# Kernel optimization log

Hardware: AMD Instinct MI355X
Metric: run time of the kernel (lower is better)

The kernel has to match this reference:

```python
import jax, jax.numpy as jnp
import numpy as np
from jax import lax

B, H, W, C, G, K = 2, 64, 64, 256, 8, 9
CQ = C // 4  # PConv partial channels
HC = C // G  # head channels
PTS = np.array([[-1, -1], [-1, 0], [-1, 1], [0, -1], [0, 0], [0, 1],
                [1, -1], [1, 0], [1, 1]], np.float32)  # (K,2) as (dx,dy)


def setup_inputs() -> dict:
    key = jax.random.key(0)
    ks = jax.random.split(key, 13)
    n = lambda i, shp, s: jax.random.normal(ks[i], shp, jnp.float32) * s
    return {
        'x': jax.random.normal(ks[0], (B, H, W, C), jnp.float32),
        'qkv_w': n(1, (C, 3 * C), C ** -0.5),
        'qkv_b': n(2, (3 * C,), 0.02),
        'dw_w': n(3, (3, 3, 1, 3 * C), 1.0 / 3.0),
        'dw_b': n(4, (3 * C,), 0.02),
        'off_pconv_w': n(5, (G, CQ, CQ, 3, 3), (CQ * 9) ** -0.5),
        'off_w': n(6, (G, 2 * K, C), 0.1 * C ** -0.5),
        'off_b': n(7, (G, 2 * K), 0.1),
        'mask_pconv_w': n(8, (CQ, CQ, 3, 3), (CQ * 9) ** -0.5),
        'mask_w': n(9, (K, C), C ** -0.5),
        'mask_b': n(10, (K,), 0.02),
        'proj_w': n(11, (C, C), C ** -0.5),
        'proj_b': n(12, (C,), 0.02),
    }


def _dwconv_nhwc(x, w, b):
    # depthwise 3x3, pad 1, stride 1; x (B,H,W,ch), w (3,3,1,ch)
    ch = x.shape[-1]
    y = lax.conv_general_dilated(x, w, (1, 1), 'SAME',
                                 dimension_numbers=('NHWC', 'HWIO', 'NHWC'),
                                 feature_group_count=ch)
    return y + b


def _pconv_nchw(x, w):
    # partial conv: 3x3 (no bias) on first CQ channels, rest untouched
    dc = w.shape[0]
    x1 = lax.conv_general_dilated(x[:, :dc], w, (1, 1), 'SAME',
                                  dimension_numbers=('NCHW', 'OIHW', 'NCHW'))
    return jnp.concatenate([x1, x[:, dc:]], axis=1)


def _flow_warp(x, flow):
    # x (N,Cc,Hh,Ww), flow (N,2K,Hh,Ww) -> (N,Cc,K,Hh,Ww)
    # bilinear grid_sample, border padding, align_corners=True == sampling at
    # absolute pixel coords with coordinate clamping.
    N, Cc, Hh, Ww = x.shape
    Kk = flow.shape[1] // 2
    fl = flow.reshape(N, Kk, 2, Hh, Ww).transpose(0, 3, 4, 1, 2)  # (N,H,W,K,2)
    gy, gx = jnp.meshgrid(jnp.arange(Hh, dtype=x.dtype),
                          jnp.arange(Ww, dtype=x.dtype), indexing='ij')
    base = jnp.stack([gx, gy], axis=-1)  # (H,W,2) in (x,y) order
    coords = base[None, :, :, None, :] + fl  # (N,H,W,K,2)
    cx = jnp.clip(coords[..., 0], 0.0, Ww - 1)
    cy = jnp.clip(coords[..., 1], 0.0, Hh - 1)
    x0 = jnp.floor(cx)
    y0 = jnp.floor(cy)
    wx = (cx - x0).reshape(N, 1, -1)
    wy = (cy - y0).reshape(N, 1, -1)
    x0i = x0.astype(jnp.int32)
    y0i = y0.astype(jnp.int32)
    x1i = jnp.minimum(x0i + 1, Ww - 1)
    y1i = jnp.minimum(y0i + 1, Hh - 1)
    xf = x.reshape(N, Cc, Hh * Ww)

    def gather(yi, xi):
        idx = (yi * Ww + xi).reshape(N, -1)  # (N, H*W*K)
        return jax.vmap(lambda im, ix: im[:, ix])(xf, idx)  # (N,Cc,H*W*K)

    v00 = gather(y0i, x0i)
    v01 = gather(y0i, x1i)
    v10 = gather(y1i, x0i)
    v11 = gather(y1i, x1i)
    out = (v00 * (1 - wx) * (1 - wy) + v01 * wx * (1 - wy)
           + v10 * (1 - wx) * wy + v11 * wx * wy)
    return out.reshape(N, Cc, Hh, Ww, Kk).transpose(0, 1, 4, 2, 3)


def reference(x, qkv_w, qkv_b, dw_w, dw_b, off_pconv_w, off_w, off_b,
              mask_pconv_w, mask_w, mask_b, proj_w, proj_b):
    Bb, Hh, Ww, Cc = x.shape
    P = Hh * Ww
    scale = HC ** -0.5
    # qkv projection + depthwise conv (NHWC)
    qkv = x @ qkv_w + qkv_b                       # (B,H,W,3C)
    qkv = _dwconv_nhwc(qkv, dw_w, dw_b)
    q = qkv[..., :Cc]                             # (B,H,W,C)
    k_map = jnp.transpose(qkv[..., Cc:2 * Cc], (0, 3, 1, 2))   # (B,C,H,W)
    v_map = jnp.transpose(qkv[..., 2 * Cc:], (0, 3, 1, 2))     # (B,C,H,W)
    q_nchw = jnp.transpose(q, (0, 3, 1, 2))

    # shared mask conv: PConv + 1x1 -> (B,K,H,W)
    xm = _pconv_nchw(q_nchw, mask_pconv_w)
    mask = jnp.einsum('bchw,oc->bohw', xm, mask_w) + mask_b[None, :, None, None]

    # base offsets per group: points_pool * (2g+1), flattened (dx,dy) pairs
    base = jnp.asarray(np.stack([(PTS * (2 * g + 1)).reshape(-1)
                                 for g in range(G)], axis=0))  # (G,2K)

    k_list, v_list = [], []
    for g in range(G):
        xo = _pconv_nchw(q_nchw, off_pconv_w[g])
        off = (jnp.einsum('bchw,oc->bohw', xo, off_w[g])
               + off_b[g][None, :, None, None]
               + base[g][None, :, None, None])  # (B,2K,H,W)
        sl = slice(g * HC, (g + 1) * HC)
        k_list.append(_flow_warp(k_map[:, sl], off) * mask[:, None])
        v_list.append(_flow_warp(v_map[:, sl], off) * mask[:, None])

    # stack (G,B,hc,K,H,W) -> (B,G,P,K,hc)
    def arrange(lst):
        t = jnp.stack(lst, axis=0).transpose(1, 0, 4, 5, 3, 2)
        return t.reshape(Bb, G, P, K, HC)

    k = arrange(k_list)
    v = arrange(v_list)
    qh = (q.reshape(Bb, Hh, Ww, G, HC).transpose(0, 3, 1, 2, 4)
          .reshape(Bb, G, P, HC)) * scale

    attn = jnp.einsum('bgpc,bgpkc->bgpk', qh, k)
    attn = jax.nn.softmax(attn, axis=-1)
    out = jnp.einsum('bgpk,bgpkc->bgpc', attn, v)       # (B,G,P,hc)
    out = out.transpose(0, 2, 1, 3).reshape(Bb, Hh, Ww, Cc)
    return out @ proj_w + proj_b
```

## Files before the change

kernel.cpp:

```cpp
#include <hip/hip_runtime.h>

typedef unsigned short u16;
typedef unsigned int u32;
typedef short bf16x8 __attribute__((ext_vector_type(8)));
typedef float f32x4 __attribute__((ext_vector_type(4)));

#define PP 4096
#define KPT 9

__device__ __forceinline__ u16 f2b(float f) {
    union { float f; unsigned int u; } v; v.f = f;
    unsigned int u = v.u;
    unsigned int r = u + 0x7FFFu + ((u >> 16) & 1u);
    return (u16)(r >> 16);
}
__device__ __forceinline__ float b2f(u16 b) {
    union { unsigned int u; float f; } v; v.u = ((unsigned int)b) << 16;
    return v.f;
}

__global__ __launch_bounds__(256) void convert_inputs(
        const float* __restrict__ x, const float* __restrict__ qkv_w,
        const float* __restrict__ proj_w,
        u16* __restrict__ x_b, u16* __restrict__ qkv_wT_b, u16* __restrict__ proj_wT_b) {
    int idx = blockIdx.x * 256 + threadIdx.x;
    if (idx < 2097152) { x_b[idx] = f2b(x[idx]); return; }
    int i2 = idx - 2097152;
    if (i2 < 196608) {
        int r = i2 / 768, c = i2 % 768;
        qkv_wT_b[c * 256 + r] = f2b(qkv_w[i2]);
        return;
    }
    int i3 = i2 - 196608;
    int r = i3 >> 8, c = i3 & 255;
    proj_wT_b[c * 256 + r] = f2b(proj_w[i3]);
}

template<bool OUT_BF16>
__global__ __launch_bounds__(256) void mfma_gemm(
        const u16* __restrict__ A, const u16* __restrict__ BT,
        const float* __restrict__ bias, void* __restrict__ out,
        int M, int N, int K) {
    __shared__ u16 As[128][40];
    __shared__ u16 Bs[64][40];
    int tid = threadIdx.x;
    int row0 = blockIdx.x * 128, col0 = blockIdx.y * 64;
    int wid = tid >> 6, lane = tid & 63;
    int wr = wid >> 1, wc = wid & 1;
    int l15 = lane & 15, lhi = lane >> 4;
    f32x4 acc[4][2] = {};
    for (int k0 = 0; k0 < K; k0 += 32) {
        #pragma unroll
        for (int q = 0; q < 2; q++) {
            int idx = tid + q * 256;
            int r = idx >> 2, kc = (idx & 3) * 8;
            *(bf16x8*)&As[r][kc] = *(const bf16x8*)&A[(size_t)(row0 + r) * K + k0 + kc];
        }
        {
            int r = tid >> 2, kc = (tid & 3) * 8;
            *(bf16x8*)&Bs[r][kc] = *(const bf16x8*)&BT[(size_t)(col0 + r) * K + k0 + kc];
        }
        __syncthreads();
        bf16x8 bfr[2];
        #pragma unroll
        for (int j = 0; j < 2; j++)
            bfr[j] = *(const bf16x8*)&Bs[wc * 32 + j * 16 + l15][lhi * 8];
        #pragma unroll
        for (int i = 0; i < 4; i++) {
            bf16x8 afr = *(const bf16x8*)&As[wr * 64 + i * 16 + l15][lhi * 8];
            #pragma unroll
            for (int j = 0; j < 2; j++)
                acc[i][j] = __builtin_amdgcn_mfma_f32_16x16x32_bf16(afr, bfr[j], acc[i][j], 0, 0, 0);
        }
        __syncthreads();
    }
    #pragma unroll
    for (int i = 0; i < 4; i++) {
        int row = row0 + wr * 64 + i * 16 + lhi * 4;
        #pragma unroll
        for (int j = 0; j < 2; j++) {
            int col = col0 + wc * 32 + j * 16 + l15;
            float bv = bias[col];
            #pragma unroll
            for (int r = 0; r < 4; r++) {
                float v = acc[i][j][r] + bv;
                if (OUT_BF16) ((u16*)out)[(size_t)(row + r) * N + col] = f2b(v);
                else          ((float*)out)[(size_t)(row + r) * N + col] = v;
            }
        }
    }
}

__global__ __launch_bounds__(256) void dwconv_b(const u16* __restrict__ qkv_b,
        const float* __restrict__ dww, const float* __restrict__ dwb,
        u16* __restrict__ out) {
    int idx = blockIdx.x * 256 + threadIdx.x;
    int c8 = (idx % 96) * 8;
    int pix = idx / 96;
    int w = pix & 63, h = (pix >> 6) & 63, b = pix >> 12;
    float acc[8];
    #pragma unroll
    for (int j = 0; j < 8; j++) acc[j] = dwb[c8 + j];
    #pragma unroll
    for (int ky = 0; ky < 3; ky++) {
        int hh = h + ky - 1;
        if (hh < 0 || hh >= 64) continue;
        #pragma unroll
        for (int kx = 0; kx < 3; kx++) {
            int ww = w + kx - 1;
            if (ww < 0 || ww >= 64) continue;
            bf16x8 v = *(const bf16x8*)&qkv_b[((size_t)((b * 64 + hh) * 64 + ww)) * 768 + c8];
            #pragma unroll
            for (int j = 0; j < 8; j++)
                acc[j] += b2f((u16)v[j]) * dww[(ky * 3 + kx) * 768 + c8 + j];
        }
    }
    bf16x8 o;
    #pragma unroll
    for (int j = 0; j < 8; j++) o[j] = (short)f2b(acc[j]);
    *(bf16x8*)&out[(size_t)idx * 8] = o;
}

__global__ void make_cw(const float* __restrict__ off_pconv_w,
        const float* __restrict__ off_w, const float* __restrict__ off_b,
        const float* __restrict__ mask_pconv_w, const float* __restrict__ mask_w,
        const float* __restrict__ mask_b, u16* __restrict__ cwT_b,
        float* __restrict__ cb) {
    int k = blockIdx.x;
    int o = threadIdx.x;
    float val = 0.f;
    if (o < 153) {
        if (k < 576) {
            int patch = k >> 6, i = k & 63;
            if (o < 144) {
                int g = o / 18, oo = o % 18;
                for (int c = 0; c < 64; c++)
                    val += off_w[(g * 18 + oo) * 256 + c] *
                           off_pconv_w[((g * 64 + c) * 64 + i) * 9 + patch];
            } else {
                int oo = o - 144;
                for (int c = 0; c < 64; c++)
                    val += mask_w[oo * 256 + c] * mask_pconv_w[(c * 64 + i) * 9 + patch];
            }
        } else {
            int j = k - 576;
            if (o < 144) {
                int g = o / 18, oo = o % 18;
                val = off_w[(g * 18 + oo) * 256 + 64 + j];
            } else {
                val = mask_w[(o - 144) * 256 + 64 + j];
            }
        }
    }
    cwT_b[o * 768 + k] = f2b(val);
    if (k == 0) {
        float bv = 0.f;
        if (o < 144) {
            int g = o / 18, oo = o % 18;
            const float PTSf[18] = {-1,-1,-1,0,-1,1,0,-1,0,0,0,1,1,-1,1,0,1,1};
            bv = off_b[g * 18 + oo] + PTSf[oo] * (float)(2 * g + 1);
        } else if (o < 153) {
            bv = mask_b[o - 144];
        }
        cb[o] = bv;
    }
}

__global__ __launch_bounds__(256) void offmask_mfma(const u16* __restrict__ qdw_b,
        const u16* __restrict__ cwT_b, const float* __restrict__ cb,
        float* __restrict__ offmask) {
    __shared__ u16 As[32][40];
    __shared__ u16 Bs[160][40];
    int tid = threadIdx.x;
    int p0 = blockIdx.x * 32;
    int wid = tid >> 6, lane = tid & 63;
    int wr = wid >> 1, wc = wid & 1;
    int l15 = lane & 15, lhi = lane >> 4;
    f32x4 acc[5] = {};
    for (int k0 = 0; k0 < 768; k0 += 32) {
        if (tid < 128) {
            int r = tid >> 2, kc = (tid & 3) * 8;
            int pixel = p0 + r;
            int w = pixel & 63, h = (pixel >> 6) & 63, b = pixel >> 12;
            bf16x8 v = {};
            if (k0 < 576) {
                int patch = k0 >> 6;
                int dy = patch / 3 - 1, dx = patch % 3 - 1;
                int hh = h + dy, ww = w + dx;
                if (hh >= 0 && hh < 64 && ww >= 0 && ww < 64)
                    v = *(const bf16x8*)&qdw_b[((size_t)((b * 64 + hh) * 64 + ww)) * 768 + (k0 & 63) + kc];
            } else {
                v = *(const bf16x8*)&qdw_b[((size_t)((b * 64 + h) * 64 + w)) * 768 + 64 + (k0 - 576) + kc];
            }
            *(bf16x8*)&As[r][kc] = v;
        }
        for (int idx = tid; idx < 640; idx += 256) {
            int r = idx >> 2, kc = (idx & 3) * 8;
            *(bf16x8*)&Bs[r][kc] = *(const bf16x8*)&cwT_b[r * 768 + k0 + kc];
        }
        __syncthreads();
        bf16x8 afr = *(const bf16x8*)&As[wr * 16 + l15][lhi * 8];
        #pragma unroll
        for (int j = 0; j < 5; j++) {
            bf16x8 bfr = *(const bf16x8*)&Bs[wc * 80 + j * 16 + l15][lhi * 8];
            acc[j] = __builtin_amdgcn_mfma_f32_16x16x32_bf16(afr, bfr, acc[j], 0, 0, 0);
        }
        __syncthreads();
    }
    int row = p0 + wr * 16 + lhi * 4;
    #pragma unroll
    for (int j = 0; j < 5; j++) {
        int col = wc * 80 + j * 16 + l15;
        float bv = cb[col];
        #pragma unroll
        for (int r = 0; r < 4; r++)
            offmask[(size_t)(row + r) * 160 + col] = acc[j][r] + bv;
    }
}

__global__ __launch_bounds__(256) void precompute_pts(const float* __restrict__ offmask,
        float4* __restrict__ pre) {
    int idx = blockIdx.x * 256 + threadIdx.x;
    if (idx >= 2 * PP * 72) return;
    int item = idx % 72;
    int pix = idx / 72;
    int g = item / 9, k = item % 9;
    int w = pix & 63, h = (pix >> 6) & 63;
    const float* om = offmask + (size_t)pix * 160;
    float dx = om[g * 18 + 2 * k];
    float dy = om[g * 18 + 2 * k + 1];
    float m  = om[144 + k];
    float cx = fminf(fmaxf((float)w + dx, 0.f), 63.f);
    float cy = fminf(fmaxf((float)h + dy, 0.f), 63.f);
    float x0f = floorf(cx), y0f = floorf(cy);
    int x0 = (int)x0f, y0 = (int)y0f;
    u32 idx00 = (u32)((pix & ~4095) | (y0 << 6) | x0);
    u32 pk = idx00 | ((x0 < 63) ? 0x10000u : 0u) | ((y0 < 63) ? 0x20000u : 0u);
    float4 o;
    o.x = __uint_as_float(pk);
    o.y = cx - x0f;
    o.z = cy - y0f;
    o.w = m;
    pre[idx] = o;
}

__global__ __launch_bounds__(256) void deform_attn(const u16* __restrict__ qdw_b,
        const float4* __restrict__ pre, u16* __restrict__ attn_b) {
    int tid = threadIdx.x;
    int unit = blockIdx.x * 16 + (tid >> 4);
    int cl = tid & 15;
    int b = unit >> 15;
    int g = (unit >> 12) & 7;
    int p = unit & 4095;
    int pix = (b << 12) | p;
    const float scale = 0.17677669529663687f;
    u32 qu = *(const u32*)&qdw_b[(size_t)pix * 768 + g * 32 + 2 * cl];
    float qlo = __uint_as_float(qu << 16) * scale;
    float qhi = __uint_as_float(qu & 0xFFFF0000u) * scale;
    const float4* pp = pre + (size_t)pix * 72 + g * 9;
    const char* base = (const char*)qdw_b;
    u32 ckb = (u32)(512 + (g * 32 + 2 * cl) * 2);
    float logit[KPT], vlo[KPT], vhi[KPT];
    #pragma unroll
    for (int k_ = 0; k_ < KPT; k_++) {
        float4 q4 = pp[k_];
        u32 pk = __float_as_uint(q4.x);
        float wx = q4.y, wy = q4.z, m = q4.w;
        u32 o00 = (pk & 0xFFFFu) * 1536u + ckb;
        u32 dX = (pk & 0x10000u) ? 1536u : 0u;
        u32 dY = (pk & 0x20000u) ? 98304u : 0u;
        u32 o01 = o00 + dX, o10 = o00 + dY, o11 = o00 + dY + dX;
        u32 k00 = *(const u32*)(base + o00);
        u32 v00 = *(const u32*)(base + o00 + 512);
        u32 k01 = *(const u32*)(base + o01);
        u32 v01 = *(const u32*)(base + o01 + 512);
        u32 k10 = *(const u32*)(base + o10);
        u32 v10 = *(const u32*)(base + o10 + 512);
        u32 k11 = *(const u32*)(base + o11);
        u32 v11 = *(const u32*)(base + o11 + 512);
        float w00 = (1.f - wx) * (1.f - wy), w01 = wx * (1.f - wy);
        float w10 = (1.f - wx) * wy,         w11 = wx * wy;
        float klo = __uint_as_float(k00 << 16) * w00 + __uint_as_float(k01 << 16) * w01
                  + __uint_as_float(k10 << 16) * w10 + __uint_as_float(k11 << 16) * w11;
        float khi = __uint_as_float(k00 & 0xFFFF0000u) * w00 + __uint_as_float(k01 & 0xFFFF0000u) * w01
                  + __uint_as_float(k10 & 0xFFFF0000u) * w10 + __uint_as_float(k11 & 0xFFFF0000u) * w11;
        float Vlo = __uint_as_float(v00 << 16) * w00 + __uint_as_float(v01 << 16) * w01
                  + __uint_as_float(v10 << 16) * w10 + __uint_as_float(v11 << 16) * w11;
        float Vhi = __uint_as_float(v00 & 0xFFFF0000u) * w00 + __uint_as_float(v01 & 0xFFFF0000u) * w01
                  + __uint_as_float(v10 & 0xFFFF0000u) * w10 + __uint_as_float(v11 & 0xFFFF0000u) * w11;
        float part = qlo * klo + qhi * khi;
        part += __shfl_xor(part, 8);
        part += __shfl_xor(part, 4);
        part += __shfl_xor(part, 2);
        part += __shfl_xor(part, 1);
        logit[k_] = part * m;
        vlo[k_] = Vlo * m;
        vhi[k_] = Vhi * m;
    }
    float mx = logit[0];
    #pragma unroll
    for (int k_ = 1; k_ < KPT; k_++) mx = fmaxf(mx, logit[k_]);
    float s = 0.f;
    #pragma unroll
    for (int k_ = 0; k_ < KPT; k_++) { logit[k_] = expf(logit[k_] - mx); s += logit[k_]; }
    float inv = 1.f / s;
    float olo = 0.f, ohi = 0.f;
    #pragma unroll
    for (int k_ = 0; k_ < KPT; k_++) { olo += logit[k_] * vlo[k_]; ohi += logit[k_] * vhi[k_]; }
    olo *= inv; ohi *= inv;
    u32 outw = (u32)f2b(olo) | ((u32)f2b(ohi) << 16);
    *(u32*)&attn_b[(size_t)pix * 256 + g * 32 + 2 * cl] = outw;
}

extern "C" void kernel_launch(void* const* d_in, const int* in_sizes, int n_in,
                              void* d_out, int out_size, void* d_ws, size_t ws_size,
                              hipStream_t stream) {
    const float* x            = (const float*)d_in[0];
    const float* qkv_w        = (const float*)d_in[1];
    const float* qkv_b        = (const float*)d_in[2];
    const float* dw_w         = (const float*)d_in[3];
    const float* dw_b         = (const float*)d_in[4];
    const float* off_pconv_w  = (const float*)d_in[5];
    const float* off_w        = (const float*)d_in[6];
    const float* off_b        = (const float*)d_in[7];
    const float* mask_pconv_w = (const float*)d_in[8];
    const float* mask_w       = (const float*)d_in[9];
    const float* mask_b       = (const float*)d_in[10];
    const float* proj_w       = (const float*)d_in[11];
    const float* proj_b       = (const float*)d_in[12];

    char* ws = (char*)d_ws;
    u16*   x_b        = (u16*)(ws);                       size_t off = 8192ull*256*2;
    u16*   qkv_wT_b   = (u16*)(ws + off);                 off += 768ull*256*2;
    u16*   proj_wT_b  = (u16*)(ws + off);                 off += 256ull*256*2;
    u16*   qkv_bf     = (u16*)(ws + off);                 off += 8192ull*768*2;
    u16*   qdw_b      = (u16*)(ws + off);                 off += 8192ull*768*2;
    u16*   cwT_b      = (u16*)(ws + off);                 off += 160ull*768*2;
    float* cb         = (float*)(ws + off);               off += 256*4;
    float* offmask    = (float*)(ws + off);               off += 8192ull*160*4;
    u16*   attn_b     = (u16*)(ws + off);                 off += 8192ull*256*2;
    float4* pre       = (float4*)(ws + off);              off += 589824ull*16;

    convert_inputs<<<9216, 256, 0, stream>>>(x, qkv_w, proj_w, x_b, qkv_wT_b, proj_wT_b);
    make_cw<<<768, 160, 0, stream>>>(off_pconv_w, off_w, off_b,
                                     mask_pconv_w, mask_w, mask_b, cwT_b, cb);
    mfma_gemm<true><<<dim3(64, 12), 256, 0, stream>>>(x_b, qkv_wT_b, qkv_b,
                                                      qkv_bf, 8192, 768, 256);
    dwconv_b<<<3072, 256, 0, stream>>>(qkv_bf, dw_w, dw_b, qdw_b);
    offmask_mfma<<<256, 256, 0, stream>>>(qdw_b, cwT_b, cb, offmask);
    precompute_pts<<<2304, 256, 0, stream>>>(offmask, pre);
    deform_attn<<<4096, 256, 0, stream>>>(qdw_b, pre, attn_b);
    mfma_gemm<false><<<dim3(64, 4), 256, 0, stream>>>(attn_b, proj_wT_b, proj_b,
                                                      d_out, 8192, 256, 256);
}
```

Before: 193.7 us.

## Fuse x fp32-to-bf16 conversion into QKV GEMM, split-K offmask, vectorize deform attention

The separate pass that converts x to bf16 is removed, and the QKV GEMM now loads fp32 activations and converts them while staging into shared memory. The offmask GEMM is split into two K-halves across twice as many blocks, writing two partial buffers that precompute_pts sums. Deform attention math is rewritten with float2 vectors to encourage packed FP32 ops. The changes cut one kernel and a global round trip and raise parallelism in offmask, at the cost of more A-load bandwidth in the GEMM (fp32 is re-read by 12 column blocks) and an extra partial-buffer write and read.

```diff
diff --git a/kernel.cpp b/kernel.cpp
--- a/kernel.cpp
+++ b/kernel.cpp
@@ -4,6 +4,7 @@
 typedef unsigned int u32;
 typedef short bf16x8 __attribute__((ext_vector_type(8)));
 typedef float f32x4 __attribute__((ext_vector_type(4)));
+typedef float f32x2 __attribute__((ext_vector_type(2)));
 
 #define PP 4096
 #define KPT 9
@@ -18,27 +19,30 @@
     union { unsigned int u; float f; } v; v.u = ((unsigned int)b) << 16;
     return v.f;
 }
+__device__ __forceinline__ f32x2 unpk2(u32 u) {
+    f32x2 r;
+    r.x = __uint_as_float(u << 16);
+    r.y = __uint_as_float(u & 0xFFFF0000u);
+    return r;
+}
 
 __global__ __launch_bounds__(256) void convert_inputs(
-        const float* __restrict__ x, const float* __restrict__ qkv_w,
-        const float* __restrict__ proj_w,
-        u16* __restrict__ x_b, u16* __restrict__ qkv_wT_b, u16* __restrict__ proj_wT_b) {
+        const float* __restrict__ qkv_w, const float* __restrict__ proj_w,
+        u16* __restrict__ qkv_wT_b, u16* __restrict__ proj_wT_b) {
     int idx = blockIdx.x * 256 + threadIdx.x;
-    if (idx < 2097152) { x_b[idx] = f2b(x[idx]); return; }
-    int i2 = idx - 2097152;
-    if (i2 < 196608) {
-        int r = i2 / 768, c = i2 % 768;
-        qkv_wT_b[c * 256 + r] = f2b(qkv_w[i2]);
+    if (idx < 196608) {
+        int r = idx / 768, c = idx % 768;
+        qkv_wT_b[c * 256 + r] = f2b(qkv_w[idx]);
         return;
     }
-    int i3 = i2 - 196608;
+    int i3 = idx - 196608;
     int r = i3 >> 8, c = i3 & 255;
     proj_wT_b[c * 256 + r] = f2b(proj_w[i3]);
 }
 
-template<bool OUT_BF16>
+template<bool OUT_BF16, bool A_F32>
 __global__ __launch_bounds__(256) void mfma_gemm(
-        const u16* __restrict__ A, const u16* __restrict__ BT,
+        const void* __restrict__ Av, const u16* __restrict__ BT,
         const float* __restrict__ bias, void* __restrict__ out,
         int M, int N, int K) {
     __shared__ u16 As[128][40];
@@ -54,7 +58,18 @@
         for (int q = 0; q < 2; q++) {
             int idx = tid + q * 256;
             int r = idx >> 2, kc = (idx & 3) * 8;
-            *(bf16x8*)&As[r][kc] = *(const bf16x8*)&A[(size_t)(row0 + r) * K + k0 + kc];
+            if (A_F32) {
+                const float* Af = (const float*)Av;
+                f32x4 a0 = *(const f32x4*)&Af[(size_t)(row0 + r) * K + k0 + kc];
+                f32x4 a1 = *(const f32x4*)&Af[(size_t)(row0 + r) * K + k0 + kc + 4];
+                bf16x8 v;
+                #pragma unroll
+                for (int j = 0; j < 4; j++) { v[j] = (short)f2b(a0[j]); v[4+j] = (short)f2b(a1[j]); }
+                *(bf16x8*)&As[r][kc] = v;
+            } else {
+                const u16* Ab = (const u16*)Av;
+                *(bf16x8*)&As[r][kc] = *(const bf16x8*)&Ab[(size_t)(row0 + r) * K + k0 + kc];
+            }
         }
         {
             int r = tid >> 2, kc = (tid & 3) * 8;
@@ -168,16 +183,19 @@
 
 __global__ __launch_bounds__(256) void offmask_mfma(const u16* __restrict__ qdw_b,
         const u16* __restrict__ cwT_b, const float* __restrict__ cb,
-        float* __restrict__ offmask) {
+        float* __restrict__ om0, float* __restrict__ om1) {
     __shared__ u16 As[32][40];
     __shared__ u16 Bs[160][40];
     int tid = threadIdx.x;
-    int p0 = blockIdx.x * 32;
+    int half = blockIdx.x & 1;
+    int p0 = (blockIdx.x >> 1) * 32;
+    int kbeg = half ? 384 : 0;
+    int kend = kbeg + 384;
     int wid = tid >> 6, lane = tid & 63;
     int wr = wid >> 1, wc = wid & 1;
     int l15 = lane & 15, lhi = lane >> 4;
     f32x4 acc[5] = {};
-    for (int k0 = 0; k0 < 768; k0 += 32) {
+    for (int k0 = kbeg; k0 < kend; k0 += 32) {
         if (tid < 128) {
             int r = tid >> 2, kc = (tid & 3) * 8;
             int pixel = p0 + r;
@@ -207,29 +225,30 @@
         }
         __syncthreads();
     }
+    float* dst = half ? om1 : om0;
     int row = p0 + wr * 16 + lhi * 4;
     #pragma unroll
     for (int j = 0; j < 5; j++) {
         int col = wc * 80 + j * 16 + l15;
-        float bv = cb[col];
+        float bv = half ? 0.f : cb[col];
         #pragma unroll
         for (int r = 0; r < 4; r++)
-            offmask[(size_t)(row + r) * 160 + col] = acc[j][r] + bv;
-    }
-}
-
-__global__ __launch_bounds__(256) void precompute_pts(const float* __restrict__ offmask,
-        float4* __restrict__ pre) {
+            dst[(size_t)(row + r) * 160 + col] = acc[j][r] + bv;
+    }
+}
+
+__global__ __launch_bounds__(256) void precompute_pts(const float* __restrict__ om0,
+        const float* __restrict__ om1, float4* __restrict__ pre) {
     int idx = blockIdx.x * 256 + threadIdx.x;
     if (idx >= 2 * PP * 72) return;
     int item = idx % 72;
     int pix = idx / 72;
     int g = item / 9, k = item % 9;
     int w = pix & 63, h = (pix >> 6) & 63;
-    const float* om = offmask + (size_t)pix * 160;
-    float dx = om[g * 18 + 2 * k];
-    float dy = om[g * 18 + 2 * k + 1];
-    float m  = om[144 + k];
+    size_t rowb = (size_t)pix * 160;
+    float dx = om0[rowb + g * 18 + 2 * k]     + om1[rowb + g * 18 + 2 * k];
+    float dy = om0[rowb + g * 18 + 2 * k + 1] + om1[rowb + g * 18 + 2 * k + 1];
+    float m  = om0[rowb + 144 + k]            + om1[rowb + 144 + k];
     float cx = fminf(fmaxf((float)w + dx, 0.f), 63.f);
     float cy = fminf(fmaxf((float)h + dy, 0.f), 63.f);
     float x0f = floorf(cx), y0f = floorf(cy);
@@ -255,12 +274,12 @@
     int pix = (b << 12) | p;
     const float scale = 0.17677669529663687f;
     u32 qu = *(const u32*)&qdw_b[(size_t)pix * 768 + g * 32 + 2 * cl];
-    float qlo = __uint_as_float(qu << 16) * scale;
-    float qhi = __uint_as_float(qu & 0xFFFF0000u) * scale;
+    f32x2 q2 = unpk2(qu) * scale;
     const float4* pp = pre + (size_t)pix * 72 + g * 9;
     const char* base = (const char*)qdw_b;
     u32 ckb = (u32)(512 + (g * 32 + 2 * cl) * 2);
-    float logit[KPT], vlo[KPT], vhi[KPT];
+    float logit[KPT];
+    f32x2 vs[KPT];
     #pragma unroll
     for (int k_ = 0; k_ < KPT; k_++) {
         float4 q4 = pp[k_];
@@ -280,22 +299,18 @@
         u32 v11 = *(const u32*)(base + o11 + 512);
         float w00 = (1.f - wx) * (1.f - wy), w01 = wx * (1.f - wy);
         float w10 = (1.f - wx) * wy,         w11 = wx * wy;
-        float klo = __uint_as_float(k00 << 16) * w00 + __uint_as_float(k01 << 16) * w01
-                  + __uint_as_float(k10 << 16) * w10 + __uint_as_float(k11 << 16) * w11;
-        float khi = __uint_as_float(k00 & 0xFFFF0000u) * w00 + __uint_as_float(k01 & 0xFFFF0000u) * w01
-                  + __uint_as_float(k10 & 0xFFFF0000u) * w10 + __uint_as_float(k11 & 0xFFFF0000u) * w11;
-        float Vlo = __uint_as_float(v00 << 16) * w00 + __uint_as_float(v01 << 16) * w01
-                  + __uint_as_float(v10 << 16) * w10 + __uint_as_float(v11 << 16) * w11;
-        float Vhi = __uint_as_float(v00 & 0xFFFF0000u) * w00 + __uint_as_float(v01 & 0xFFFF0000u) * w01
-                  + __uint_as_float(v10 & 0xFFFF0000u) * w10 + __uint_as_float(v11 & 0xFFFF0000u) * w11;
-        float part = qlo * klo + qhi * khi;
+        f32x2 kk = unpk2(k00) * w00 + unpk2(k01) * w01
+                 + unpk2(k10) * w10 + unpk2(k11) * w11;
+        f32x2 vv = unpk2(v00) * w00 + unpk2(v01) * w01
+                 + unpk2(v10) * w10 + unpk2(v11) * w11;
+        f32x2 pr = q2 * kk;
+        float part = pr.x + pr.y;
         part += __shfl_xor(part, 8);
         part += __shfl_xor(part, 4);
         part += __shfl_xor(part, 2);
         part += __shfl_xor(part, 1);
         logit[k_] = part * m;
-        vlo[k_] = Vlo * m;
-        vhi[k_] = Vhi * m;
+        vs[k_] = vv * m;
     }
     float mx = logit[0];
     #pragma unroll
@@ -304,11 +319,11 @@
     #pragma unroll
     for (int k_ = 0; k_ < KPT; k_++) { logit[k_] = expf(logit[k_] - mx); s += logit[k_]; }
     float inv = 1.f / s;
-    float olo = 0.f, ohi = 0.f;
-    #pragma unroll
-    for (int k_ = 0; k_ < KPT; k_++) { olo += logit[k_] * vlo[k_]; ohi += logit[k_] * vhi[k_]; }
-    olo *= inv; ohi *= inv;
-    u32 outw = (u32)f2b(olo) | ((u32)f2b(ohi) << 16);
+    f32x2 o2 = {0.f, 0.f};
+    #pragma unroll
+    for (int k_ = 0; k_ < KPT; k_++) o2 += vs[k_] * logit[k_];
+    o2 *= inv;
+    u32 outw = (u32)f2b(o2.x) | ((u32)f2b(o2.y) << 16);
     *(u32*)&attn_b[(size_t)pix * 256 + g * 32 + 2 * cl] = outw;
 }
 
@@ -330,26 +345,27 @@
     const float* proj_b       = (const float*)d_in[12];
 
     char* ws = (char*)d_ws;
-    u16*   x_b        = (u16*)(ws);                       size_t off = 8192ull*256*2;
+    size_t off = 0;
     u16*   qkv_wT_b   = (u16*)(ws + off);                 off += 768ull*256*2;
     u16*   proj_wT_b  = (u16*)(ws + off);                 off += 256ull*256*2;
     u16*   qkv_bf     = (u16*)(ws + off);                 off += 8192ull*768*2;
     u16*   qdw_b      = (u16*)(ws + off);                 off += 8192ull*768*2;
     u16*   cwT_b      = (u16*)(ws + off);                 off += 160ull*768*2;
     float* cb         = (float*)(ws + off);               off += 256*4;
-    float* offmask    = (float*)(ws + off);               off += 8192ull*160*4;
+    float* om0        = (float*)(ws + off);               off += 8192ull*160*4;
+    float* om1        = (float*)(ws + off);               off += 8192ull*160*4;
     u16*   attn_b     = (u16*)(ws + off);                 off += 8192ull*256*2;
     float4* pre       = (float4*)(ws + off);              off += 589824ull*16;
 
-    convert_inputs<<<9216, 256, 0, stream>>>(x, qkv_w, proj_w, x_b, qkv_wT_b, proj_wT_b);
+    convert_inputs<<<1024, 256, 0, stream>>>(qkv_w, proj_w, qkv_wT_b, proj_wT_b);
     make_cw<<<768, 160, 0, stream>>>(off_pconv_w, off_w, off_b,
                                      mask_pconv_w, mask_w, mask_b, cwT_b, cb);
-    mfma_gemm<true><<<dim3(64, 12), 256, 0, stream>>>(x_b, qkv_wT_b, qkv_b,
-                                                      qkv_bf, 8192, 768, 256);
+    mfma_gemm<true, true><<<dim3(64, 12), 256, 0, stream>>>(x, qkv_wT_b, qkv_b,
+                                                            qkv_bf, 8192, 768, 256);
     dwconv_b<<<3072, 256, 0, stream>>>(qkv_bf, dw_w, dw_b, qdw_b);
-    offmask_mfma<<<256, 256, 0, stream>>>(qdw_b, cwT_b, cb, offmask);
-    precompute_pts<<<2304, 256, 0, stream>>>(offmask, pre);
+    offmask_mfma<<<512, 256, 0, stream>>>(qdw_b, cwT_b, cb, om0, om1);
+    precompute_pts<<<2304, 256, 0, stream>>>(om0, om1, pre);
     deform_attn<<<4096, 256, 0, stream>>>(qdw_b, pre, attn_b);
-    mfma_gemm<false><<<dim3(64, 4), 256, 0, stream>>>(attn_b, proj_wT_b, proj_b,
-                                                      d_out, 8192, 256, 256);
-}
+    mfma_gemm<false, false><<<dim3(64, 4), 256, 0, stream>>>(attn_b, proj_wT_b, proj_b,
+                                                             d_out, 8192, 256, 256);
+}
```

Measured after the change: 173.2 us. 1.12x faster.
